# Kernel optimization log

Measured on AMD Instinct MI355X. Metric: run time of the kernel, lower is better.

Reference implementation:

```python
import jax, jax.numpy as jnp
import numpy as np

DIM = 1024
HEADS = 16


def setup_inputs() -> dict:
    key = jax.random.key(0)
    k1, k2, k3, k4 = jax.random.split(key, 4)
    x = jax.random.normal(k1, (4, 2048, DIM), dtype=jnp.float32)
    s = 1.0 / np.sqrt(DIM)
    w_qkv = jax.random.normal(k2, (DIM, 3 * DIM), dtype=jnp.float32) * s
    w_out = jax.random.normal(k3, (DIM, DIM), dtype=jnp.float32) * s
    b_out = jax.random.normal(k4, (DIM,), dtype=jnp.float32) * 0.01
    return {"x": x, "w_qkv": w_qkv, "w_out": w_out, "b_out": b_out}


def reference(x, w_qkv, w_out, b_out):
    b, n, d = x.shape
    h = HEADS
    dh = d // h
    scale = dh ** -0.5
    qkv = x @ w_qkv  # [b, n, 3d]
    q, k, v = jnp.split(qkv, 3, axis=-1)
    # [b, n, d] -> [b, h, n, dh]
    def to_heads(t):
        return t.reshape(b, n, h, dh).transpose(0, 2, 1, 3)
    q, k, v = to_heads(q), to_heads(k), to_heads(v)
    dots = jnp.einsum('bhid,bhjd->bhij', q, k) * scale
    attn = jax.nn.softmax(dots, axis=-1)
    out = jnp.einsum('bhij,bhjd->bhid', attn, v)
    out = out.transpose(0, 2, 1, 3).reshape(b, n, d)
    return out @ w_out + b_out
```

## Files before the change

kernel.cpp:

```cpp
#include <hip/hip_runtime.h>
#include <hip/hip_bf16.h>


typedef __attribute__((ext_vector_type(4))) float f32x4;
typedef __attribute__((ext_vector_type(16))) float f32x16;
typedef __attribute__((ext_vector_type(8))) unsigned short u16x8;
typedef __attribute__((ext_vector_type(4))) unsigned short u16x4;
typedef __attribute__((ext_vector_type(4))) unsigned int u32x4;
typedef __attribute__((ext_vector_type(8))) __bf16 bf16x8;

static __device__ __forceinline__ f32x4 mfma_bf16(u16x8 a, u16x8 b, f32x4 c) {
    return __builtin_amdgcn_mfma_f32_16x16x32_bf16(
        __builtin_bit_cast(bf16x8, a), __builtin_bit_cast(bf16x8, b), c, 0, 0, 0);
}
static __device__ __forceinline__ f32x16 mfma32(u16x8 a, u16x8 b, f32x16 c) {
    return __builtin_amdgcn_mfma_f32_32x32x16_bf16(
        __builtin_bit_cast(bf16x8, a), __builtin_bit_cast(bf16x8, b), c, 0, 0, 0);
}

static __device__ __forceinline__ unsigned short f2bf(float f) {
    unsigned int u = __builtin_bit_cast(unsigned int, f);
    u += 0x7fffu + ((u >> 16) & 1u);
    return (unsigned short)(u >> 16);
}
static __device__ __forceinline__ unsigned int cvt_pk_bf16(float a, float b) {
    unsigned int r;
    asm("v_cvt_pk_bf16_f32 %0, %1, %2" : "=v"(r) : "v"(a), "v"(b));
    return r;
}
static __device__ __forceinline__ float fexp2(float x) {
    float r;
    asm("v_exp_f32 %0, %1" : "=v"(r) : "v"(x));
    return r;
}
static __device__ __forceinline__ float frcp(float x) {
    float r;
    asm("v_rcp_f32 %0, %1" : "=v"(r) : "v"(x));
    return r;
}
typedef const __attribute__((address_space(1))) unsigned int* gp1_t;
typedef __attribute__((address_space(3))) unsigned int* lp3_t;
static __device__ __forceinline__ void gl_lds16(const void* g, void* l) {
    __builtin_amdgcn_global_load_lds((gp1_t)g, (lp3_t)l, 16, 0, 0);
}

__global__ void k_cvt(const float* __restrict__ in, unsigned short* __restrict__ out, int n4) {
    int i = blockIdx.x * blockDim.x + threadIdx.x;
    int stride = gridDim.x * blockDim.x;
    for (; i < n4; i += stride) {
        f32x4 v = ((const f32x4*)in)[i];
        u16x4 o;
        #pragma unroll
        for (int j = 0; j < 4; ++j) o[j] = f2bf(v[j]);
        ((u16x4*)out)[i] = o;
    }
}

__global__ void k_transpose(const float* __restrict__ in, unsigned short* __restrict__ out,
                            int R, int C) {
    __shared__ float tile[32][33];
    int c0 = blockIdx.x * 32, r0 = blockIdx.y * 32;
    int tx = threadIdx.x, ty = threadIdx.y;
    #pragma unroll
    for (int i = ty; i < 32; i += 8)
        tile[i][tx] = in[(size_t)(r0 + i) * C + c0 + tx];
    __syncthreads();
    #pragma unroll
    for (int i = ty; i < 32; i += 8)
        out[(size_t)(c0 + i) * R + r0 + tx] = f2bf(tile[tx][i]);
}

__global__ __launch_bounds__(512, 2) void k_gemm1(
    const unsigned short* __restrict__ A,
    const unsigned short* __restrict__ BT,
    unsigned short* __restrict__ Qs,
    unsigned short* __restrict__ Ks,
    unsigned short* __restrict__ VTs)
{
    __shared__ unsigned short As[2][256 * 64];
    __shared__ unsigned short Bs[2][256 * 64];
    const int K = 1024;
    const int tid = threadIdx.x, lane = tid & 63, wave = tid >> 6;

    int lin = blockIdx.y * 12 + blockIdx.x;
    int xcd = lin & 7, idx = lin >> 3;
    int virt = xcd * 48 + idx;
    int by = virt & 31, bx = virt >> 5;
    const int m0 = by * 256, n0 = bx * 256;

    const int wm = (wave >> 2) * 128, wn = (wave & 3) * 64;
    const int lr = lane & 15, half = lane >> 4;
    const int srow = lane >> 3, sslot = lane & 7;

    auto stage = [&](int buf, int t) {
        int k0 = t * 64;
        #pragma unroll
        for (int r = 0; r < 4; ++r) {
            int chunk = r * 8 + wave;
            int row = chunk * 8 + srow;
            int koff = (sslot ^ (row & 7)) * 8;
            gl_lds16(&A[(size_t)(m0 + row) * K + k0 + koff], &As[buf][chunk * 512]);
        }
        #pragma unroll
        for (int r = 0; r < 4; ++r) {
            int chunk = r * 8 + wave;
            int row = chunk * 8 + srow;
            int koff = (sslot ^ (row & 7)) * 8;
            gl_lds16(&BT[(size_t)(n0 + row) * K + k0 + koff], &Bs[buf][chunk * 512]);
        }
    };

    f32x4 acc[8][4] = {};

    stage(0, 0);
    asm volatile("s_waitcnt vmcnt(0)" ::: "memory");
    __builtin_amdgcn_s_barrier();

    for (int t = 0; t < 16; ++t) {
        const int cur = t & 1;
        if (t < 15) stage(cur ^ 1, t + 1);
        const unsigned short* Ab = As[cur];
        const unsigned short* Bb = Bs[cur];

        u16x8 bfr[4];
        #pragma unroll
        for (int q = 0; q < 4; ++q) {
            const int ks = q >> 1, ih = q & 1;
            if (ih == 0) {
                #pragma unroll
                for (int j = 0; j < 4; ++j) {
                    int rb = wn + j * 16 + lr;
                    bfr[j] = *(const u16x8*)&Bb[rb * 64 + (((ks * 4 + half) ^ (rb & 7)) * 8)];
                }
            }
            u16x8 af[4];
            #pragma unroll
            for (int ii = 0; ii < 4; ++ii) {
                int ra = wm + (ih * 4 + ii) * 16 + lr;
                af[ii] = *(const u16x8*)&Ab[ra * 64 + (((ks * 4 + half) ^ (ra & 7)) * 8)];
            }
            asm volatile("s_waitcnt lgkmcnt(0)" ::: "memory");
            __builtin_amdgcn_sched_barrier(0);
            __builtin_amdgcn_s_setprio(1);
            #pragma unroll
            for (int ii = 0; ii < 4; ++ii)
                #pragma unroll
                for (int j = 0; j < 4; ++j)
                    acc[ih * 4 + ii][j] = mfma_bf16(af[ii], bfr[j], acc[ih * 4 + ii][j]);
            __builtin_amdgcn_s_setprio(0);
        }

        if (t < 15) asm volatile("s_waitcnt vmcnt(0)" ::: "memory");
        __builtin_amdgcn_s_barrier();
    }

    #pragma unroll
    for (int i = 0; i < 8; ++i) {
        int rowb = m0 + wm + i * 16 + half * 4;
        int b = rowb >> 11, n = rowb & 2047;
        int bh16 = (b << 4);
        #pragma unroll
        for (int j = 0; j < 4; ++j) {
            int col = n0 + wn + j * 16 + lr;
            int part = col >> 10, cj = col & 1023;
            int h = cj >> 6, d = cj & 63;
            int bh = bh16 + h;
            if (part == 0) {
                #pragma unroll
                for (int r = 0; r < 4; ++r)
                    Qs[((size_t)bh * 2048 + n + r) * 64 + d] = f2bf(acc[i][j][r] * 0.18033688f);
            } else if (part == 1) {
                #pragma unroll
                for (int r = 0; r < 4; ++r)
                    Ks[((size_t)bh * 2048 + n + r) * 64 + d] = f2bf(acc[i][j][r]);
            } else {
                u16x4 p;
                #pragma unroll
                for (int r = 0; r < 4; ++r) p[r] = f2bf(acc[i][j][r]);
                *(u16x4*)&VTs[((size_t)bh * 64 + d) * 2048 + n] = p;
            }
        }
    }
}

__global__ __launch_bounds__(512, 1) void k_gemm2(
    const unsigned short* __restrict__ A,
    const unsigned short* __restrict__ BT,
    const float* __restrict__ bias,
    float* __restrict__ outf)
{
    __shared__ unsigned short As[3][256 * 64];
    __shared__ unsigned short Bs[3][128 * 64];
    const int K = 1024;
    const int tid = threadIdx.x, lane = tid & 63, wave = tid >> 6;

    int gx = gridDim.x;
    int nwg = gx * gridDim.y;
    int lin = blockIdx.y * gx + blockIdx.x;
    int virt = (lin & 7) * (nwg >> 3) + (lin >> 3);
    int bx = virt % gx, by = virt / gx;
    const int m0 = by * 256, n0 = bx * 128;

    const int wm = (wave >> 1) * 64, wn = (wave & 1) * 64;
    const int lr = lane & 15, half = lane >> 4;
    const int srow = lane >> 3, sslot = lane & 7;

    auto stage_sub = [&](int buf, int t, int h) {
        int k0 = t * 64;
        #pragma unroll
        for (int r = 0; r < 2; ++r) {
            int chunk = (h * 2 + r) * 8 + wave;
            int row = chunk * 8 + srow;
            int koff = (sslot ^ (row & 7)) * 8;
            gl_lds16(&A[(size_t)(m0 + row) * K + k0 + koff], &As[buf][chunk * 512]);
        }
        {
            int chunk = h * 8 + wave;
            int row = chunk * 8 + srow;
            int koff = (sslot ^ (row & 7)) * 8;
            gl_lds16(&BT[(size_t)(n0 + row) * K + k0 + koff], &Bs[buf][chunk * 512]);
        }
    };

    f32x4 acc[4][4] = {};

    stage_sub(0, 0, 0); stage_sub(0, 0, 1);
    stage_sub(1, 1, 0); stage_sub(1, 1, 1);
    asm volatile("s_waitcnt vmcnt(6)" ::: "memory");
    __builtin_amdgcn_s_barrier();

    for (int t = 0; t < 16; ++t) {
        const int cur = t % 3, nxt = (t + 2) % 3;
        const bool do_stage = (t + 2) < 16;
        const unsigned short* Ab = As[cur];
        const unsigned short* Bb = Bs[cur];

        #pragma unroll
        for (int ks = 0; ks < 2; ++ks) {
            u16x8 af[4], bfr[4];
            #pragma unroll
            for (int i = 0; i < 4; ++i) {
                int ra = wm + i * 16 + lr;
                af[i] = *(const u16x8*)&Ab[ra * 64 + (((ks * 4 + half) ^ (ra & 7)) * 8)];
                int rb = wn + i * 16 + lr;
                bfr[i] = *(const u16x8*)&Bb[rb * 64 + (((ks * 4 + half) ^ (rb & 7)) * 8)];
            }
            if (do_stage) stage_sub(nxt, t + 2, ks);
            if (ks == 1) {
                if (t < 14)       asm volatile("s_waitcnt vmcnt(6)" ::: "memory");
                else if (t == 14) asm volatile("s_waitcnt vmcnt(0)" ::: "memory");
            }
            __builtin_amdgcn_s_barrier();
            asm volatile("s_waitcnt lgkmcnt(0)" ::: "memory");
            __builtin_amdgcn_sched_barrier(0);
            __builtin_amdgcn_s_setprio(1);
            #pragma unroll
            for (int i = 0; i < 4; ++i)
                #pragma unroll
                for (int j = 0; j < 4; ++j)
                    acc[i][j] = mfma_bf16(af[i], bfr[j], acc[i][j]);
            __builtin_amdgcn_s_setprio(0);
            __builtin_amdgcn_s_barrier();
        }
    }

    #pragma unroll
    for (int i = 0; i < 4; ++i)
        #pragma unroll
        for (int j = 0; j < 4; ++j)
            #pragma unroll
            for (int r = 0; r < 4; ++r) {
                int row = m0 + wm + i * 16 + half * 4 + r;
                int col = n0 + wn + j * 16 + lr;
                outf[(size_t)row * 1024 + col] = acc[i][j][r] + bias[col];
            }
}

__global__ __launch_bounds__(256, 2) void k_attn(
    const unsigned short* __restrict__ Qs,
    const unsigned short* __restrict__ Ks,
    const unsigned short* __restrict__ VTs,
    unsigned short* __restrict__ attn)
{
    __shared__ unsigned short Kt[2][64 * 64];
    __shared__ unsigned short Vt[2][64 * 64];
    const int tid = threadIdx.x, lane = tid & 63, wave = tid >> 6;

    int lin = blockIdx.y * 8 + blockIdx.x;
    int virt = (lin & 7) * 64 + (lin >> 3);
    int bh = virt >> 3;
    int q0 = (virt & 7) * 256 + wave * 64;

    const int lq = lane & 31;
    const int hi = lane >> 5;
    const bool hib = hi != 0;

    const unsigned short* Kbase = Ks + (size_t)bh * 2048 * 64;
    const unsigned short* Vbase = VTs + (size_t)bh * 64 * 2048;

    u16x8 qf0[4], qf1[4];
    {
        const unsigned short* Qr0 = Qs + ((size_t)bh * 2048 + q0 + lq) * 64;
        const unsigned short* Qr1 = Qr0 + 32 * 64;
        #pragma unroll
        for (int kk = 0; kk < 4; ++kk) {
            qf0[kk] = *(const u16x8*)&Qr0[kk * 16 + hi * 8];
            qf1[kk] = *(const u16x8*)&Qr1[kk * 16 + hi * 8];
        }
    }

    const int srow_in = lane >> 4, sslot = lane & 15;
    auto stage = [&](int buf, int j0) {
        #pragma unroll
        for (int c = 0; c < 2; ++c) {
            int chunk = wave * 2 + c;
            int row = chunk * 4 + srow_in;
            int v = sslot ^ (row & 15);
            int high = v >> 3, dsl = (v & 7) * 8;
            gl_lds16(Kbase + (size_t)(j0 + high * 32 + row) * 64 + dsl, &Kt[buf][chunk * 512]);
            gl_lds16(Vbase + (size_t)(high * 32 + row) * 2048 + j0 + dsl, &Vt[buf][chunk * 512]);
        }
    };

    f32x16 o0[2] = {}, o1[2] = {};
    f32x16 osum0 = {}, osum1 = {};
    const u16x8 onesf = {0x3F80, 0x3F80, 0x3F80, 0x3F80, 0x3F80, 0x3F80, 0x3F80, 0x3F80};

    stage(0, 0);
    __syncthreads();
    int cur = 0;

    for (int t = 0; t < 32; ++t) {
        if (t < 31) stage(cur ^ 1, (t + 1) * 64);

        f32x16 sacc0[2] = {}, sacc1[2] = {};
        __builtin_amdgcn_s_setprio(1);
        #pragma unroll
        for (int jb = 0; jb < 2; ++jb) {
            u16x8 kf[4];
            #pragma unroll
            for (int kk = 0; kk < 4; ++kk) {
                int s = (jb * 8 + kk * 2 + hi) ^ (lq & 15);
                kf[kk] = *(const u16x8*)&Kt[cur][lq * 128 + s * 8];
            }
            #pragma unroll
            for (int kk = 0; kk < 4; ++kk) sacc0[jb] = mfma32(kf[kk], qf0[kk], sacc0[jb]);
            #pragma unroll
            for (int kk = 0; kk < 4; ++kk) sacc1[jb] = mfma32(kf[kk], qf1[kk], sacc1[jb]);
        }
        __builtin_amdgcn_s_setprio(0);

        unsigned int pk0[16], pk1[16];
        #pragma unroll
        for (int jb = 0; jb < 2; ++jb)
            #pragma unroll
            for (int i = 0; i < 8; ++i) {
                pk0[jb * 8 + i] = cvt_pk_bf16(fexp2(sacc0[jb][2 * i]), fexp2(sacc0[jb][2 * i + 1]));
                pk1[jb * 8 + i] = cvt_pk_bf16(fexp2(sacc1[jb][2 * i]), fexp2(sacc1[jb][2 * i + 1]));
            }

        #pragma unroll
        for (int kk = 0; kk < 4; ++kk) {
            const int base = (kk >> 1) * 8 + (kk & 1) * 4;
            unsigned int a0 = pk0[base + 0], a1 = pk0[base + 1], a2 = pk0[base + 2], a3 = pk0[base + 3];
            unsigned int b0 = pk1[base + 0], b1 = pk1[base + 1], b2 = pk1[base + 2], b3 = pk1[base + 3];
            unsigned int sa0 = __shfl_xor(a0, 32), sa1 = __shfl_xor(a1, 32);
            unsigned int sa2 = __shfl_xor(a2, 32), sa3 = __shfl_xor(a3, 32);
            unsigned int sb0 = __shfl_xor(b0, 32), sb1 = __shfl_xor(b1, 32);
            unsigned int sb2 = __shfl_xor(b2, 32), sb3 = __shfl_xor(b3, 32);
            u32x4 w0, w1;
            w0[0] = hib ? sa2 : a0;  w0[1] = hib ? sa3 : a1;
            w0[2] = hib ? a2 : sa0;  w0[3] = hib ? a3 : sa1;
            w1[0] = hib ? sb2 : b0;  w1[1] = hib ? sb3 : b1;
            w1[2] = hib ? b2 : sb0;  w1[3] = hib ? b3 : sb1;
            u16x8 pa0 = __builtin_bit_cast(u16x8, w0);
            u16x8 pa1 = __builtin_bit_cast(u16x8, w1);
            __builtin_amdgcn_s_setprio(1);
            osum0 = mfma32(pa0, onesf, osum0);
            osum1 = mfma32(pa1, onesf, osum1);
            #pragma unroll
            for (int db = 0; db < 2; ++db) {
                int s = (db * 8 + kk * 2 + hi) ^ (lq & 15);
                u16x8 vf = *(const u16x8*)&Vt[cur][lq * 128 + s * 8];
                o0[db] = mfma32(pa0, vf, o0[db]);
                o1[db] = mfma32(pa1, vf, o1[db]);
            }
            __builtin_amdgcn_s_setprio(0);
        }

        __syncthreads();
        cur ^= 1;
    }

    int b = bh >> 4, h = bh & 15;
    #pragma unroll
    for (int r = 0; r < 16; ++r) {
        int qrow = (r & 3) + 8 * (r >> 2) + 4 * hi;
        float i0 = frcp(osum0[r]);
        float i1 = frcp(osum1[r]);
        size_t ro0 = (size_t)(b * 2048 + q0 + qrow) * 1024 + h * 64;
        size_t ro1 = (size_t)(b * 2048 + q0 + 32 + qrow) * 1024 + h * 64;
        attn[ro0 + lq]      = f2bf(o0[0][r] * i0);
        attn[ro0 + 32 + lq] = f2bf(o0[1][r] * i0);
        attn[ro1 + lq]      = f2bf(o1[0][r] * i1);
        attn[ro1 + 32 + lq] = f2bf(o1[1][r] * i1);
    }
}

extern "C" void kernel_launch(void* const* d_in, const int* in_sizes, int n_in,
                              void* d_out, int out_size, void* d_ws, size_t ws_size,
                              hipStream_t stream) {
    const float* x     = (const float*)d_in[0];
    const float* w_qkv = (const float*)d_in[1];
    const float* w_out = (const float*)d_in[2];
    const float* b_out = (const float*)d_in[3];
    float* out = (float*)d_out;

    char* ws = (char*)d_ws;
    size_t off = 0;
    auto alloc = [&](size_t bytes) -> void* {
        void* p = ws + off;
        off += (bytes + 255) & ~(size_t)255;
        return p;
    };
    unsigned short* xb    = (unsigned short*)alloc(8192ull * 1024 * 2);
    unsigned short* wqkvT = (unsigned short*)alloc(3072ull * 1024 * 2);
    unsigned short* woutT = (unsigned short*)alloc(1024ull * 1024 * 2);
    unsigned short* Qs    = (unsigned short*)alloc(64ull * 2048 * 64 * 2);
    unsigned short* Ks    = (unsigned short*)alloc(64ull * 2048 * 64 * 2);
    unsigned short* VTs   = (unsigned short*)alloc(64ull * 2048 * 64 * 2);
    unsigned short* attn  = (unsigned short*)alloc(8192ull * 1024 * 2);
    if (off > ws_size) return;

    k_cvt<<<2048, 256, 0, stream>>>(x, xb, 8192 * 1024 / 4);
    k_transpose<<<dim3(3072 / 32, 1024 / 32), dim3(32, 8), 0, stream>>>(w_qkv, wqkvT, 1024, 3072);
    k_transpose<<<dim3(1024 / 32, 1024 / 32), dim3(32, 8), 0, stream>>>(w_out, woutT, 1024, 1024);
    k_gemm1<<<dim3(12, 32), 512, 0, stream>>>(xb, wqkvT, Qs, Ks, VTs);
    k_attn<<<dim3(8, 64), 256, 0, stream>>>(Qs, Ks, VTs, attn);
    k_gemm2<<<dim3(8, 32), 512, 0, stream>>>(attn, woutT, b_out, out);
}
```

Measured before the change: 209.2 us.

## Shrink QKV GEMM and attention tiles for more blocks and occupancy

The QKV projection GEMM moves from 256x256 tiles with BK=64 and 512 threads to 128x128 tiles with BK=32 and 256 threads, using a new LDS swizzle and plain __syncthreads. The attention kernel drops from two 32-row query groups per wave to one, doubling the grid and raising the occupancy target. Both changes aim for more concurrent waves and better latency hiding across the CUs. The cost is less data reuse per block, more global and LDS traffic, and more barriers per unit of work.

```diff
diff --git a/kernel.cpp b/kernel.cpp
--- a/kernel.cpp
+++ b/kernel.cpp
@@ -70,92 +70,72 @@
         out[(size_t)(c0 + i) * R + r0 + tx] = f2bf(tile[tx][i]);
 }
 
-__global__ __launch_bounds__(512, 2) void k_gemm1(
+__global__ __launch_bounds__(256, 4) void k_gemm1(
     const unsigned short* __restrict__ A,
     const unsigned short* __restrict__ BT,
     unsigned short* __restrict__ Qs,
     unsigned short* __restrict__ Ks,
     unsigned short* __restrict__ VTs)
 {
-    __shared__ unsigned short As[2][256 * 64];
-    __shared__ unsigned short Bs[2][256 * 64];
+    __shared__ unsigned short As[2][128 * 32];
+    __shared__ unsigned short Bs[2][128 * 32];
     const int K = 1024;
     const int tid = threadIdx.x, lane = tid & 63, wave = tid >> 6;
 
-    int lin = blockIdx.y * 12 + blockIdx.x;
+    int lin = blockIdx.y * 24 + blockIdx.x;
     int xcd = lin & 7, idx = lin >> 3;
-    int virt = xcd * 48 + idx;
-    int by = virt & 31, bx = virt >> 5;
-    const int m0 = by * 256, n0 = bx * 256;
-
-    const int wm = (wave >> 2) * 128, wn = (wave & 3) * 64;
+    int virt = xcd * 192 + idx;
+    int bx = virt >> 6, by = virt & 63;
+    const int m0 = by * 128, n0 = bx * 128;
+
+    const int wm = (wave >> 1) * 64, wn = (wave & 1) * 64;
     const int lr = lane & 15, half = lane >> 4;
-    const int srow = lane >> 3, sslot = lane & 7;
-
+
+    const int srow_in = lane >> 2, sslot = lane & 3;
     auto stage = [&](int buf, int t) {
-        int k0 = t * 64;
-        #pragma unroll
-        for (int r = 0; r < 4; ++r) {
-            int chunk = r * 8 + wave;
-            int row = chunk * 8 + srow;
-            int koff = (sslot ^ (row & 7)) * 8;
-            gl_lds16(&A[(size_t)(m0 + row) * K + k0 + koff], &As[buf][chunk * 512]);
-        }
-        #pragma unroll
-        for (int r = 0; r < 4; ++r) {
-            int chunk = r * 8 + wave;
-            int row = chunk * 8 + srow;
-            int koff = (sslot ^ (row & 7)) * 8;
-            gl_lds16(&BT[(size_t)(n0 + row) * K + k0 + koff], &Bs[buf][chunk * 512]);
+        int k0 = t * 32;
+        #pragma unroll
+        for (int c = 0; c < 2; ++c) {
+            int chunk = wave * 2 + c;
+            int row = chunk * 16 + srow_in;
+            int gk = (sslot ^ ((row >> 1) & 3)) * 8;
+            gl_lds16(&A[(size_t)(m0 + row) * K + k0 + gk], &As[buf][chunk * 512]);
+            gl_lds16(&BT[(size_t)(n0 + row) * K + k0 + gk], &Bs[buf][chunk * 512]);
         }
     };
 
-    f32x4 acc[8][4] = {};
+    f32x4 acc[4][4] = {};
 
     stage(0, 0);
-    asm volatile("s_waitcnt vmcnt(0)" ::: "memory");
-    __builtin_amdgcn_s_barrier();
-
-    for (int t = 0; t < 16; ++t) {
+    __syncthreads();
+
+    for (int t = 0; t < 32; ++t) {
         const int cur = t & 1;
-        if (t < 15) stage(cur ^ 1, t + 1);
+        if (t < 31) stage(cur ^ 1, t + 1);
         const unsigned short* Ab = As[cur];
         const unsigned short* Bb = Bs[cur];
 
-        u16x8 bfr[4];
-        #pragma unroll
-        for (int q = 0; q < 4; ++q) {
-            const int ks = q >> 1, ih = q & 1;
-            if (ih == 0) {
-                #pragma unroll
-                for (int j = 0; j < 4; ++j) {
-                    int rb = wn + j * 16 + lr;
-                    bfr[j] = *(const u16x8*)&Bb[rb * 64 + (((ks * 4 + half) ^ (rb & 7)) * 8)];
-                }
-            }
-            u16x8 af[4];
-            #pragma unroll
-            for (int ii = 0; ii < 4; ++ii) {
-                int ra = wm + (ih * 4 + ii) * 16 + lr;
-                af[ii] = *(const u16x8*)&Ab[ra * 64 + (((ks * 4 + half) ^ (ra & 7)) * 8)];
-            }
-            asm volatile("s_waitcnt lgkmcnt(0)" ::: "memory");
-            __builtin_amdgcn_sched_barrier(0);
-            __builtin_amdgcn_s_setprio(1);
-            #pragma unroll
-            for (int ii = 0; ii < 4; ++ii)
-                #pragma unroll
-                for (int j = 0; j < 4; ++j)
-                    acc[ih * 4 + ii][j] = mfma_bf16(af[ii], bfr[j], acc[ih * 4 + ii][j]);
-            __builtin_amdgcn_s_setprio(0);
-        }
-
-        if (t < 15) asm volatile("s_waitcnt vmcnt(0)" ::: "memory");
-        __builtin_amdgcn_s_barrier();
+        u16x8 af[4], bfr[4];
+        #pragma unroll
+        for (int i = 0; i < 4; ++i) {
+            int ra = wm + i * 16 + lr;
+            af[i] = *(const u16x8*)&Ab[ra * 32 + ((half ^ ((ra >> 1) & 3)) * 8)];
+            int rb = wn + i * 16 + lr;
+            bfr[i] = *(const u16x8*)&Bb[rb * 32 + ((half ^ ((rb >> 1) & 3)) * 8)];
+        }
+        __builtin_amdgcn_s_setprio(1);
+        #pragma unroll
+        for (int i = 0; i < 4; ++i)
+            #pragma unroll
+            for (int j = 0; j < 4; ++j)
+                acc[i][j] = mfma_bf16(af[i], bfr[j], acc[i][j]);
+        __builtin_amdgcn_s_setprio(0);
+
+        __syncthreads();
     }
 
     #pragma unroll
-    for (int i = 0; i < 8; ++i) {
+    for (int i = 0; i < 4; ++i) {
         int rowb = m0 + wm + i * 16 + half * 4;
         int b = rowb >> 11, n = rowb & 2047;
         int bh16 = (b << 4);
@@ -276,7 +256,7 @@
             }
 }
 
-__global__ __launch_bounds__(256, 2) void k_attn(
+__global__ __launch_bounds__(256, 4) void k_attn(
     const unsigned short* __restrict__ Qs,
     const unsigned short* __restrict__ Ks,
     const unsigned short* __restrict__ VTs,
@@ -286,10 +266,10 @@
     __shared__ unsigned short Vt[2][64 * 64];
     const int tid = threadIdx.x, lane = tid & 63, wave = tid >> 6;
 
-    int lin = blockIdx.y * 8 + blockIdx.x;
-    int virt = (lin & 7) * 64 + (lin >> 3);
-    int bh = virt >> 3;
-    int q0 = (virt & 7) * 256 + wave * 64;
+    int lin = blockIdx.y * 16 + blockIdx.x;
+    int virt = (lin & 7) * 128 + (lin >> 3);
+    int bh = virt >> 4;
+    int q0 = (virt & 15) * 128 + wave * 32;
 
     const int lq = lane & 31;
     const int hi = lane >> 5;
@@ -298,15 +278,12 @@
     const unsigned short* Kbase = Ks + (size_t)bh * 2048 * 64;
     const unsigned short* Vbase = VTs + (size_t)bh * 64 * 2048;
 
-    u16x8 qf0[4], qf1[4];
+    u16x8 qf[4];
     {
-        const unsigned short* Qr0 = Qs + ((size_t)bh * 2048 + q0 + lq) * 64;
-        const unsigned short* Qr1 = Qr0 + 32 * 64;
-        #pragma unroll
-        for (int kk = 0; kk < 4; ++kk) {
-            qf0[kk] = *(const u16x8*)&Qr0[kk * 16 + hi * 8];
-            qf1[kk] = *(const u16x8*)&Qr1[kk * 16 + hi * 8];
-        }
+        const unsigned short* Qr = Qs + ((size_t)bh * 2048 + q0 + lq) * 64;
+        #pragma unroll
+        for (int kk = 0; kk < 4; ++kk)
+            qf[kk] = *(const u16x8*)&Qr[kk * 16 + hi * 8];
     }
 
     const int srow_in = lane >> 4, sslot = lane & 15;
@@ -322,8 +299,8 @@
         }
     };
 
-    f32x16 o0[2] = {}, o1[2] = {};
-    f32x16 osum0 = {}, osum1 = {};
+    f32x16 o[2] = {};
+    f32x16 osum = {};
     const u16x8 onesf = {0x3F80, 0x3F80, 0x3F80, 0x3F80, 0x3F80, 0x3F80, 0x3F80, 0x3F80};
 
     stage(0, 0);
@@ -333,7 +310,7 @@
     for (int t = 0; t < 32; ++t) {
         if (t < 31) stage(cur ^ 1, (t + 1) * 64);
 
-        f32x16 sacc0[2] = {}, sacc1[2] = {};
+        f32x16 sacc[2] = {};
         __builtin_amdgcn_s_setprio(1);
         #pragma unroll
         for (int jb = 0; jb < 2; ++jb) {
@@ -344,46 +321,35 @@
                 kf[kk] = *(const u16x8*)&Kt[cur][lq * 128 + s * 8];
             }
             #pragma unroll
-            for (int kk = 0; kk < 4; ++kk) sacc0[jb] = mfma32(kf[kk], qf0[kk], sacc0[jb]);
-            #pragma unroll
-            for (int kk = 0; kk < 4; ++kk) sacc1[jb] = mfma32(kf[kk], qf1[kk], sacc1[jb]);
+            for (int kk = 0; kk < 4; ++kk)
+                sacc[jb] = mfma32(kf[kk], qf[kk], sacc[jb]);
         }
         __builtin_amdgcn_s_setprio(0);
 
-        unsigned int pk0[16], pk1[16];
+        unsigned int pk[16];
         #pragma unroll
         for (int jb = 0; jb < 2; ++jb)
             #pragma unroll
-            for (int i = 0; i < 8; ++i) {
-                pk0[jb * 8 + i] = cvt_pk_bf16(fexp2(sacc0[jb][2 * i]), fexp2(sacc0[jb][2 * i + 1]));
-                pk1[jb * 8 + i] = cvt_pk_bf16(fexp2(sacc1[jb][2 * i]), fexp2(sacc1[jb][2 * i + 1]));
-            }
+            for (int i = 0; i < 8; ++i)
+                pk[jb * 8 + i] = cvt_pk_bf16(fexp2(sacc[jb][2 * i]), fexp2(sacc[jb][2 * i + 1]));
 
         #pragma unroll
         for (int kk = 0; kk < 4; ++kk) {
             const int base = (kk >> 1) * 8 + (kk & 1) * 4;
-            unsigned int a0 = pk0[base + 0], a1 = pk0[base + 1], a2 = pk0[base + 2], a3 = pk0[base + 3];
-            unsigned int b0 = pk1[base + 0], b1 = pk1[base + 1], b2 = pk1[base + 2], b3 = pk1[base + 3];
+            unsigned int a0 = pk[base + 0], a1 = pk[base + 1], a2 = pk[base + 2], a3 = pk[base + 3];
             unsigned int sa0 = __shfl_xor(a0, 32), sa1 = __shfl_xor(a1, 32);
             unsigned int sa2 = __shfl_xor(a2, 32), sa3 = __shfl_xor(a3, 32);
-            unsigned int sb0 = __shfl_xor(b0, 32), sb1 = __shfl_xor(b1, 32);
-            unsigned int sb2 = __shfl_xor(b2, 32), sb3 = __shfl_xor(b3, 32);
-            u32x4 w0, w1;
+            u32x4 w0;
             w0[0] = hib ? sa2 : a0;  w0[1] = hib ? sa3 : a1;
             w0[2] = hib ? a2 : sa0;  w0[3] = hib ? a3 : sa1;
-            w1[0] = hib ? sb2 : b0;  w1[1] = hib ? sb3 : b1;
-            w1[2] = hib ? b2 : sb0;  w1[3] = hib ? b3 : sb1;
-            u16x8 pa0 = __builtin_bit_cast(u16x8, w0);
-            u16x8 pa1 = __builtin_bit_cast(u16x8, w1);
+            u16x8 pa = __builtin_bit_cast(u16x8, w0);
             __builtin_amdgcn_s_setprio(1);
-            osum0 = mfma32(pa0, onesf, osum0);
-            osum1 = mfma32(pa1, onesf, osum1);
+            osum = mfma32(pa, onesf, osum);
             #pragma unroll
             for (int db = 0; db < 2; ++db) {
                 int s = (db * 8 + kk * 2 + hi) ^ (lq & 15);
                 u16x8 vf = *(const u16x8*)&Vt[cur][lq * 128 + s * 8];
-                o0[db] = mfma32(pa0, vf, o0[db]);
-                o1[db] = mfma32(pa1, vf, o1[db]);
+                o[db] = mfma32(pa, vf, o[db]);
             }
             __builtin_amdgcn_s_setprio(0);
         }
@@ -396,14 +362,10 @@
     #pragma unroll
     for (int r = 0; r < 16; ++r) {
         int qrow = (r & 3) + 8 * (r >> 2) + 4 * hi;
-        float i0 = frcp(osum0[r]);
-        float i1 = frcp(osum1[r]);
-        size_t ro0 = (size_t)(b * 2048 + q0 + qrow) * 1024 + h * 64;
-        size_t ro1 = (size_t)(b * 2048 + q0 + 32 + qrow) * 1024 + h * 64;
-        attn[ro0 + lq]      = f2bf(o0[0][r] * i0);
-        attn[ro0 + 32 + lq] = f2bf(o0[1][r] * i0);
-        attn[ro1 + lq]      = f2bf(o1[0][r] * i1);
-        attn[ro1 + 32 + lq] = f2bf(o1[1][r] * i1);
+        float invr = frcp(osum[r]);
+        size_t ro = (size_t)(b * 2048 + q0 + qrow) * 1024 + h * 64;
+        attn[ro + lq]      = f2bf(o[0][r] * invr);
+        attn[ro + 32 + lq] = f2bf(o[1][r] * invr);
     }
 }
 
@@ -435,7 +397,7 @@
     k_cvt<<<2048, 256, 0, stream>>>(x, xb, 8192 * 1024 / 4);
     k_transpose<<<dim3(3072 / 32, 1024 / 32), dim3(32, 8), 0, stream>>>(w_qkv, wqkvT, 1024, 3072);
     k_transpose<<<dim3(1024 / 32, 1024 / 32), dim3(32, 8), 0, stream>>>(w_out, woutT, 1024, 1024);
-    k_gemm1<<<dim3(12, 32), 512, 0, stream>>>(xb, wqkvT, Qs, Ks, VTs);
-    k_attn<<<dim3(8, 64), 256, 0, stream>>>(Qs, Ks, VTs, attn);
+    k_gemm1<<<dim3(24, 64), 256, 0, stream>>>(xb, wqkvT, Qs, Ks, VTs);
+    k_attn<<<dim3(16, 64), 256, 0, stream>>>(Qs, Ks, VTs, attn);
     k_gemm2<<<dim3(8, 32), 512, 0, stream>>>(attn, woutT, b_out, out);
 }
```

After: 208.4 us. About the same (-0.4%).
